# Optimization experiments

Hardware: AMD Instinct MI355X
Metric: run time of the kernel (lower is better)

The kernel has to match this reference:

```python
import jax, jax.numpy as jnp
import numpy as np

B, N, D, E, FF, K = 2, 1024, 768, 8, 4, 2
H = D * FF  # 3072


def _xavier_uniform(key, shape, gain=1.0):
    # shape is (..., out, in) like torch Linear weight; fan_in/out from last two dims
    fan_out, fan_in = shape[-2], shape[-1]
    limit = gain * np.sqrt(6.0 / (fan_in + fan_out))
    return jax.random.uniform(key, shape, jnp.float32, -limit, limit)


def setup_inputs() -> dict:
    key = jax.random.key(0)
    ks = jax.random.split(key, 5)
    tokens = jax.random.normal(ks[0], (B, N, D), jnp.float32)
    # Token-choice top-K routing: softmax over experts, keep top-K weights
    logits = jax.random.normal(ks[1], (B, N, E), jnp.float32)
    probs = jax.nn.softmax(logits, axis=-1)
    topv, topi = jax.lax.top_k(probs, K)              # (B,N,K)
    onehot = jax.nn.one_hot(topi, E, dtype=jnp.float32)  # (B,N,K,E)
    combine_weights = jnp.einsum('bnk,bnke->bne', topv, onehot)  # (B,N,E)
    dispatch_weights = (combine_weights > 0).astype(jnp.float32)
    # Stacked expert weights (torch Linear convention: W is (out, in), y = x @ W.T)
    Wg = _xavier_uniform(ks[2], (E, H, D))
    Wv = _xavier_uniform(ks[3], (E, H, D))
    Wo = _xavier_uniform(ks[4], (E, D, H), gain=0.02)
    scale = jnp.full((E,), 1.0 / E, jnp.float32)  # output_scale init = 1/E
    return dict(tokens=tokens, dispatch_weights=dispatch_weights,
                combine_weights=combine_weights, Wg=Wg, Wv=Wv, Wo=Wo, scale=scale)


def reference(tokens, dispatch_weights, combine_weights, Wg, Wv, Wo, scale):
    Bb, Nn, Dd = tokens.shape
    Ee = Wg.shape[0]
    x = tokens.reshape(Bb * Nn, Dd)                    # (T, D)
    mask = (dispatch_weights.reshape(-1, Ee) > 0).astype(x.dtype)  # (T, E)
    comb = combine_weights.reshape(-1, Ee) * mask      # zero where not dispatched
    # SwiGLU-style expert FFN, all experts in one grouped contraction
    gate = jax.nn.gelu(jnp.einsum('td,ehd->teh', x, Wg), approximate=False)  # (T,E,H)
    value = jnp.einsum('td,ehd->teh', x, Wv)           # (T,E,H)
    expert_out = jnp.einsum('teh,edh->ted', gate * value, Wo) * scale[None, :, None]  # (T,E,D)
    # Weighted combine: sum_e comb[t,e] * expert_out[t,e,:]
    y = jnp.einsum('ted,te->td', expert_out, comb)     # (T, D)
    return y.reshape(Bb, Nn, Dd)
```

## Files before the change

### kernel.cpp

```cpp
#include <hip/hip_runtime.h>
#include <hip/hip_bf16.h>
#include <math.h>

#define T_TOK 2048
#define DIM   768
#define NEXP  8
#define HDIM  3072
#define MAXP  (T_TOK * 2)
#define LDST  40
#define NTILE_MAX 40

typedef __attribute__((ext_vector_type(8))) short bfrag;
typedef __attribute__((ext_vector_type(4))) float f32x4;

__device__ __forceinline__ unsigned short f2bf(float f) {
  union { float f; unsigned int u; } x; x.f = f;
  unsigned int r = x.u + 0x7fffu + ((x.u >> 16) & 1u);
  return (unsigned short)(r >> 16);
}

__global__ void k_route(const float* __restrict__ disp,
                        const float* __restrict__ comb,
                        int* __restrict__ meta,
                        float* __restrict__ row_comb,
                        int* __restrict__ row_token,
                        int* __restrict__ tok2pair) {
  __shared__ int s_cnt[NEXP], s_off[NEXP], s_cur[NEXP];
  __shared__ int s_tn[T_TOK];
  int tid = threadIdx.x;
  if (tid < NEXP) s_cnt[tid] = 0;
  for (int t = tid; t < T_TOK; t += 256) s_tn[t] = 0;
  __syncthreads();
  for (int t = tid; t < T_TOK; t += 256)
    for (int e = 0; e < NEXP; ++e)
      if (disp[t * NEXP + e] > 0.f) atomicAdd(&s_cnt[e], 1);
  __syncthreads();
  if (tid == 0) {
    int acc = 0;
    for (int e = 0; e < NEXP; ++e) { s_off[e] = acc; acc += s_cnt[e]; }
  }
  __syncthreads();
  if (tid < NEXP) {
    s_cur[tid] = s_off[tid];
    meta[tid] = s_cnt[tid];
    meta[NEXP + tid] = s_off[tid];
  }
  __syncthreads();
  for (int t = tid; t < T_TOK; t += 256)
    for (int e = 0; e < NEXP; ++e)
      if (disp[t * NEXP + e] > 0.f) {
        int p = atomicAdd(&s_cur[e], 1);
        row_token[p] = t;
        row_comb[p] = comb[t * NEXP + e];
        int sl = atomicAdd(&s_tn[t], 1);
        tok2pair[t * 2 + sl] = p;
      }
  __syncthreads();
  if (tid == 0) {
    int nt = 0;
    for (int e = 0; e < NEXP; ++e)
      for (int m0 = 0; m0 < s_cnt[e]; m0 += 128)
        meta[17 + nt++] = (e << 16) | (m0 >> 7);
    meta[16] = nt;
  }
}

__global__ void k_xbf(const float* __restrict__ X, unsigned short* __restrict__ Xb) {
  size_t i = ((size_t)blockIdx.x * 256 + threadIdx.x) * 8;
  float4 a = *(const float4*)(X + i);
  float4 b = *(const float4*)(X + i + 4);
  unsigned short r[8];
  r[0]=f2bf(a.x); r[1]=f2bf(a.y); r[2]=f2bf(a.z); r[3]=f2bf(a.w);
  r[4]=f2bf(b.x); r[5]=f2bf(b.y); r[6]=f2bf(b.z); r[7]=f2bf(b.w);
  *(uint4*)(Xb + i) = *(uint4*)r;
}

__global__ __launch_bounds__(256, 2) void k_gemm_gv(
    const unsigned short* __restrict__ Xb,
    const float* __restrict__ Wg,
    const float* __restrict__ Wv,
    const int* __restrict__ meta,
    const int* __restrict__ row_token,
    unsigned short* __restrict__ ubuf)
{
  int blk = blockIdx.x;
  int t = blk % NTILE_MAX;
  int nt = blk / NTILE_MAX;
  if (t >= meta[16]) return;
  int tv = meta[17 + t];
  int e = tv >> 16, m0 = (tv & 0xffff) << 7;
  int cnt = meta[e], off = meta[NEXP + e];
  int n0 = nt * 128;

  __shared__ unsigned short As[128 * LDST];
  __shared__ unsigned short Bgs[128 * LDST];
  __shared__ unsigned short Bvs[128 * LDST];

  int tid = threadIdx.x;
  int wid = tid >> 6, lane = tid & 63;
  int wm = (wid >> 1) * 64, wn = (wid & 1) * 64;
  int lr = lane & 15, quad = lane >> 4;

  int a_tok[2];
#pragma unroll
  for (int r = 0; r < 2; ++r) {
    int row = (tid + 256 * r) >> 2;
    int gr = m0 + row; if (gr >= cnt) gr = cnt - 1;
    a_tok[r] = row_token[off + gr];
  }

  const float* Wgb = Wg + (size_t)e * ((size_t)HDIM * DIM);
  const float* Wvb = Wv + (size_t)e * ((size_t)HDIM * DIM);

  f32x4 zero4 = {0.f, 0.f, 0.f, 0.f};
  f32x4 accg[4][4], accv[4][4];
#pragma unroll
  for (int i = 0; i < 4; ++i)
#pragma unroll
    for (int j = 0; j < 4; ++j) { accg[i][j] = zero4; accv[i][j] = zero4; }

  for (int k0 = 0; k0 < DIM; k0 += 32) {
    __syncthreads();
#pragma unroll
    for (int r = 0; r < 2; ++r) {
      int c = tid + 256 * r;
      int row = c >> 2, sub = c & 3;
      uint4 av = *(const uint4*)(Xb + (size_t)a_tok[r] * DIM + k0 + sub * 8);
      *(uint4*)(&As[row * LDST + sub * 8]) = av;
    }
#pragma unroll
    for (int r = 0; r < 4; ++r) {
      int c = tid + 256 * r;
      int row = c >> 3, c4 = c & 7;
      float4 gv = *(const float4*)(Wgb + (size_t)(n0 + row) * DIM + k0 + c4 * 4);
      ushort4 gp;
      gp.x = f2bf(gv.x); gp.y = f2bf(gv.y); gp.z = f2bf(gv.z); gp.w = f2bf(gv.w);
      *(ushort4*)(&Bgs[row * LDST + c4 * 4]) = gp;
      float4 vv = *(const float4*)(Wvb + (size_t)(n0 + row) * DIM + k0 + c4 * 4);
      ushort4 vp;
      vp.x = f2bf(vv.x); vp.y = f2bf(vv.y); vp.z = f2bf(vv.z); vp.w = f2bf(vv.w);
      *(ushort4*)(&Bvs[row * LDST + c4 * 4]) = vp;
    }
    __syncthreads();
    bfrag a[4], bg[4], bv[4];
#pragma unroll
    for (int i = 0; i < 4; ++i)
      a[i] = *(const bfrag*)(&As[(wm + i * 16 + lr) * LDST + quad * 8]);
#pragma unroll
    for (int j = 0; j < 4; ++j) {
      bg[j] = *(const bfrag*)(&Bgs[(wn + j * 16 + lr) * LDST + quad * 8]);
      bv[j] = *(const bfrag*)(&Bvs[(wn + j * 16 + lr) * LDST + quad * 8]);
    }
#pragma unroll
    for (int i = 0; i < 4; ++i)
#pragma unroll
      for (int j = 0; j < 4; ++j) {
        accg[i][j] = __builtin_amdgcn_mfma_f32_16x16x32_bf16(a[i], bg[j], accg[i][j], 0, 0, 0);
        accv[i][j] = __builtin_amdgcn_mfma_f32_16x16x32_bf16(a[i], bv[j], accv[i][j], 0, 0, 0);
      }
  }

#pragma unroll
  for (int i = 0; i < 4; ++i)
#pragma unroll
    for (int rg = 0; rg < 4; ++rg) {
      int gr = m0 + wm + i * 16 + quad * 4 + rg;
      if (gr < cnt) {
        size_t base = (size_t)(off + gr) * HDIM + n0 + wn;
#pragma unroll
        for (int j = 0; j < 4; ++j) {
          float g = accg[i][j][rg];
          float v = accv[i][j][rg];
          float u = 0.5f * g * (1.0f + erff(g * 0.70710678118654752f)) * v;
          ubuf[base + j * 16 + lr] = f2bf(u);
        }
      }
    }
}

__global__ __launch_bounds__(256, 2) void k_gemm_out(
    const unsigned short* __restrict__ U,
    const float* __restrict__ Wo,
    const float* __restrict__ scale,
    const int* __restrict__ meta,
    const int* __restrict__ row_token,
    const float* __restrict__ row_comb,
    float* __restrict__ partial,
    float* __restrict__ out,
    int mode)
{
  int blk = blockIdx.x;
  int t = blk % NTILE_MAX;
  int rest = blk / NTILE_MAX;
  int nt = rest % 6;
  int ks = rest / 6;
  if (t >= meta[16]) return;
  int tv = meta[17 + t];
  int e = tv >> 16, m0 = (tv & 0xffff) << 7;
  int cnt = meta[e], off = meta[NEXP + e];
  int n0 = nt * 128;
  int kbase = ks * (HDIM / 4);

  __shared__ unsigned short As[128 * LDST];
  __shared__ unsigned short Bs[128 * LDST];

  int tid = threadIdx.x;
  int wid = tid >> 6, lane = tid & 63;
  int wm = (wid >> 1) * 64, wn = (wid & 1) * 64;
  int lr = lane & 15, quad = lane >> 4;

  int a_grow[2];
#pragma unroll
  for (int r = 0; r < 2; ++r) {
    int row = (tid + 256 * r) >> 2;
    int gr = m0 + row; if (gr >= cnt) gr = cnt - 1;
    a_grow[r] = off + gr;
  }

  const float* Wb = Wo + (size_t)e * ((size_t)DIM * HDIM);

  f32x4 zero4 = {0.f, 0.f, 0.f, 0.f};
  f32x4 acc[4][4];
#pragma unroll
  for (int i = 0; i < 4; ++i)
#pragma unroll
    for (int j = 0; j < 4; ++j) acc[i][j] = zero4;

  for (int kk = 0; kk < HDIM / 4; kk += 32) {
    int k0 = kbase + kk;
    __syncthreads();
#pragma unroll
    for (int r = 0; r < 2; ++r) {
      int c = tid + 256 * r;
      int row = c >> 2, sub = c & 3;
      uint4 av = *(const uint4*)(U + (size_t)a_grow[r] * HDIM + k0 + sub * 8);
      *(uint4*)(&As[row * LDST + sub * 8]) = av;
    }
#pragma unroll
    for (int r = 0; r < 4; ++r) {
      int c = tid + 256 * r;
      int row = c >> 3, c4 = c & 7;
      float4 bvv = *(const float4*)(Wb + (size_t)(n0 + row) * HDIM + k0 + c4 * 4);
      ushort4 bp;
      bp.x = f2bf(bvv.x); bp.y = f2bf(bvv.y); bp.z = f2bf(bvv.z); bp.w = f2bf(bvv.w);
      *(ushort4*)(&Bs[row * LDST + c4 * 4]) = bp;
    }
    __syncthreads();
    bfrag a[4], b[4];
#pragma unroll
    for (int i = 0; i < 4; ++i)
      a[i] = *(const bfrag*)(&As[(wm + i * 16 + lr) * LDST + quad * 8]);
#pragma unroll
    for (int j = 0; j < 4; ++j)
      b[j] = *(const bfrag*)(&Bs[(wn + j * 16 + lr) * LDST + quad * 8]);
#pragma unroll
    for (int i = 0; i < 4; ++i)
#pragma unroll
      for (int j = 0; j < 4; ++j)
        acc[i][j] = __builtin_amdgcn_mfma_f32_16x16x32_bf16(a[i], b[j], acc[i][j], 0, 0, 0);
  }

  float sc = scale[e];
#pragma unroll
  for (int i = 0; i < 4; ++i)
#pragma unroll
    for (int rg = 0; rg < 4; ++rg) {
      int gr = m0 + wm + i * 16 + quad * 4 + rg;
      if (gr < cnt) {
        int grow = off + gr;
        float w = row_comb[grow] * sc;
        if (mode == 0) {
          float* pb = partial + ((size_t)ks * MAXP + grow) * DIM + n0 + wn;
#pragma unroll
          for (int j = 0; j < 4; ++j)
            pb[j * 16 + lr] = acc[i][j][rg] * w;
        } else {
          int tok = row_token[grow];
          float* ob = out + (size_t)tok * DIM + n0 + wn;
#pragma unroll
          for (int j = 0; j < 4; ++j)
            atomicAdd(ob + j * 16 + lr, acc[i][j][rg] * w);
        }
      }
    }
}

__global__ void k_combine(const float* __restrict__ partial,
                          const int* __restrict__ tok2pair,
                          float* __restrict__ out) {
  int idx = blockIdx.x * 256 + threadIdx.x;
  int t = idx / 192, d4 = idx % 192;
  int p0 = tok2pair[t * 2], p1 = tok2pair[t * 2 + 1];
  float sx = 0.f, sy = 0.f, sz = 0.f, sw = 0.f;
#pragma unroll
  for (int ks = 0; ks < 4; ++ks) {
    float4 a = *(const float4*)(partial + ((size_t)ks * MAXP + p0) * DIM + d4 * 4);
    float4 b = *(const float4*)(partial + ((size_t)ks * MAXP + p1) * DIM + d4 * 4);
    sx += a.x + b.x; sy += a.y + b.y; sz += a.z + b.z; sw += a.w + b.w;
  }
  float4 r; r.x = sx; r.y = sy; r.z = sz; r.w = sw;
  *(float4*)(out + (size_t)t * DIM + d4 * 4) = r;
}

extern "C" void kernel_launch(void* const* d_in, const int* in_sizes, int n_in,
                              void* d_out, int out_size, void* d_ws, size_t ws_size,
                              hipStream_t stream) {
  const float* tokens = (const float*)d_in[0];
  const float* disp   = (const float*)d_in[1];
  const float* comb   = (const float*)d_in[2];
  const float* Wg     = (const float*)d_in[3];
  const float* Wv     = (const float*)d_in[4];
  const float* Wo     = (const float*)d_in[5];
  const float* scale  = (const float*)d_in[6];
  float* out = (float*)d_out;

  char* ws = (char*)d_ws;
  int*   meta      = (int*)ws;
  int*   row_token = (int*)(ws + 16384);
  float* row_comb  = (float*)(ws + 32768);
  int*   tok2pair  = (int*)(ws + 49152);
  unsigned short* Xb   = (unsigned short*)(ws + (1u << 20));
  unsigned short* ubuf = (unsigned short*)(ws + (5u << 20));
  float* partial = (float*)(ws + (32ull << 20));
  size_t need_partial = (32ull << 20) + (size_t)4 * MAXP * DIM * sizeof(float);
  int mode = (ws_size >= need_partial) ? 0 : 1;

  hipLaunchKernelGGL(k_route, dim3(1), dim3(256), 0, stream,
                     disp, comb, meta, row_comb, row_token, tok2pair);
  hipLaunchKernelGGL(k_xbf, dim3((T_TOK * DIM) / (256 * 8)), dim3(256), 0, stream,
                     tokens, Xb);
  hipLaunchKernelGGL(k_gemm_gv, dim3(NTILE_MAX * 24), dim3(256), 0, stream,
                     Xb, Wg, Wv, meta, row_token, ubuf);
  if (mode == 1)
    hipMemsetAsync(d_out, 0, (size_t)out_size * sizeof(float), stream);
  hipLaunchKernelGGL(k_gemm_out, dim3(NTILE_MAX * 6 * 4), dim3(256), 0, stream,
                     ubuf, Wo, scale, meta, row_token, row_comb, partial, out, mode);
  if (mode == 0)
    hipLaunchKernelGGL(k_combine, dim3((T_TOK * DIM / 4) / 256), dim3(256), 0, stream,
                       partial, tok2pair, out);
}
```

Measured before the change: 422.7 us.

## Pre-convert expert weights to bf16 and stage GEMM tiles with async LDS loads

```diff
diff --git a/kernel.cpp b/kernel.cpp
--- a/kernel.cpp
+++ b/kernel.cpp
@@ -17,6 +17,12 @@
   union { float f; unsigned int u; } x; x.f = f;
   unsigned int r = x.u + 0x7fffu + ((x.u >> 16) & 1u);
   return (unsigned short)(r >> 16);
+}
+
+__device__ __forceinline__ void async16(const void* g, void* l) {
+  __builtin_amdgcn_global_load_lds(
+      (const __attribute__((address_space(1))) void*)g,
+      (__attribute__((address_space(3))) void*)l, 16, 0, 0);
 }
 
 __global__ void k_route(const float* __restrict__ disp,
@@ -65,20 +71,30 @@
   }
 }
 
-__global__ void k_xbf(const float* __restrict__ X, unsigned short* __restrict__ Xb) {
-  size_t i = ((size_t)blockIdx.x * 256 + threadIdx.x) * 8;
-  float4 a = *(const float4*)(X + i);
-  float4 b = *(const float4*)(X + i + 4);
+#define CH_X   196608
+#define CH_W   2359296
+__global__ void k_cvt(const float* __restrict__ X, const float* __restrict__ Wg,
+                      const float* __restrict__ Wv, const float* __restrict__ Wo,
+                      unsigned short* __restrict__ Xb, unsigned short* __restrict__ Wgb,
+                      unsigned short* __restrict__ Wvb, unsigned short* __restrict__ Wob) {
+  int c = blockIdx.x * 256 + threadIdx.x;
+  const float* src; unsigned short* dst; size_t idx;
+  if (c < CH_X)                { src = X;  dst = Xb;  idx = (size_t)c * 8; }
+  else if (c < CH_X + CH_W)    { src = Wg; dst = Wgb; idx = (size_t)(c - CH_X) * 8; }
+  else if (c < CH_X + 2*CH_W)  { src = Wv; dst = Wvb; idx = (size_t)(c - CH_X - CH_W) * 8; }
+  else                         { src = Wo; dst = Wob; idx = (size_t)(c - CH_X - 2*CH_W) * 8; }
+  float4 a = *(const float4*)(src + idx);
+  float4 b = *(const float4*)(src + idx + 4);
   unsigned short r[8];
   r[0]=f2bf(a.x); r[1]=f2bf(a.y); r[2]=f2bf(a.z); r[3]=f2bf(a.w);
   r[4]=f2bf(b.x); r[5]=f2bf(b.y); r[6]=f2bf(b.z); r[7]=f2bf(b.w);
-  *(uint4*)(Xb + i) = *(uint4*)r;
-}
-
-__global__ __launch_bounds__(256, 2) void k_gemm_gv(
+  *(uint4*)(dst + idx) = *(uint4*)r;
+}
+
+__global__ __launch_bounds__(256, 2) void k_gemm_gv_a(
     const unsigned short* __restrict__ Xb,
-    const float* __restrict__ Wg,
-    const float* __restrict__ Wv,
+    const unsigned short* __restrict__ Wgb,
+    const unsigned short* __restrict__ Wvb,
     const int* __restrict__ meta,
     const int* __restrict__ row_token,
     unsigned short* __restrict__ ubuf)
@@ -92,25 +108,26 @@
   int cnt = meta[e], off = meta[NEXP + e];
   int n0 = nt * 128;
 
-  __shared__ unsigned short As[128 * LDST];
-  __shared__ unsigned short Bgs[128 * LDST];
-  __shared__ unsigned short Bvs[128 * LDST];
+  __shared__ unsigned short As[128 * 32];
+  __shared__ unsigned short Bgs[128 * 32];
+  __shared__ unsigned short Bvs[128 * 32];
 
   int tid = threadIdx.x;
   int wid = tid >> 6, lane = tid & 63;
   int wm = (wid >> 1) * 64, wn = (wid & 1) * 64;
   int lr = lane & 15, quad = lane >> 4;
 
-  int a_tok[2];
+  int a_tok[2]; int sub[2]; int brow[2];
 #pragma unroll
   for (int r = 0; r < 2; ++r) {
-    int row = (tid + 256 * r) >> 2;
+    int c = tid + 256 * r;
+    int row = c >> 2; sub[r] = c & 3; brow[r] = row;
     int gr = m0 + row; if (gr >= cnt) gr = cnt - 1;
     a_tok[r] = row_token[off + gr];
   }
 
-  const float* Wgb = Wg + (size_t)e * ((size_t)HDIM * DIM);
-  const float* Wvb = Wv + (size_t)e * ((size_t)HDIM * DIM);
+  const unsigned short* WgB = Wgb + (size_t)e * HDIM * DIM;
+  const unsigned short* WvB = Wvb + (size_t)e * HDIM * DIM;
 
   f32x4 zero4 = {0.f, 0.f, 0.f, 0.f};
   f32x4 accg[4][4], accv[4][4];
@@ -124,32 +141,19 @@
 #pragma unroll
     for (int r = 0; r < 2; ++r) {
       int c = tid + 256 * r;
-      int row = c >> 2, sub = c & 3;
-      uint4 av = *(const uint4*)(Xb + (size_t)a_tok[r] * DIM + k0 + sub * 8);
-      *(uint4*)(&As[row * LDST + sub * 8]) = av;
-    }
-#pragma unroll
-    for (int r = 0; r < 4; ++r) {
-      int c = tid + 256 * r;
-      int row = c >> 3, c4 = c & 7;
-      float4 gv = *(const float4*)(Wgb + (size_t)(n0 + row) * DIM + k0 + c4 * 4);
-      ushort4 gp;
-      gp.x = f2bf(gv.x); gp.y = f2bf(gv.y); gp.z = f2bf(gv.z); gp.w = f2bf(gv.w);
-      *(ushort4*)(&Bgs[row * LDST + c4 * 4]) = gp;
-      float4 vv = *(const float4*)(Wvb + (size_t)(n0 + row) * DIM + k0 + c4 * 4);
-      ushort4 vp;
-      vp.x = f2bf(vv.x); vp.y = f2bf(vv.y); vp.z = f2bf(vv.z); vp.w = f2bf(vv.w);
-      *(ushort4*)(&Bvs[row * LDST + c4 * 4]) = vp;
+      async16(Xb + (size_t)a_tok[r] * DIM + k0 + sub[r] * 8, &As[c * 8]);
+      async16(WgB + (size_t)(n0 + brow[r]) * DIM + k0 + sub[r] * 8, &Bgs[c * 8]);
+      async16(WvB + (size_t)(n0 + brow[r]) * DIM + k0 + sub[r] * 8, &Bvs[c * 8]);
     }
     __syncthreads();
     bfrag a[4], bg[4], bv[4];
 #pragma unroll
     for (int i = 0; i < 4; ++i)
-      a[i] = *(const bfrag*)(&As[(wm + i * 16 + lr) * LDST + quad * 8]);
+      a[i] = *(const bfrag*)(&As[(wm + i * 16 + lr) * 32 + quad * 8]);
 #pragma unroll
     for (int j = 0; j < 4; ++j) {
-      bg[j] = *(const bfrag*)(&Bgs[(wn + j * 16 + lr) * LDST + quad * 8]);
-      bv[j] = *(const bfrag*)(&Bvs[(wn + j * 16 + lr) * LDST + quad * 8]);
+      bg[j] = *(const bfrag*)(&Bgs[(wn + j * 16 + lr) * 32 + quad * 8]);
+      bv[j] = *(const bfrag*)(&Bvs[(wn + j * 16 + lr) * 32 + quad * 8]);
     }
 #pragma unroll
     for (int i = 0; i < 4; ++i)
@@ -178,16 +182,13 @@
     }
 }
 
-__global__ __launch_bounds__(256, 2) void k_gemm_out(
+__global__ __launch_bounds__(256, 2) void k_gemm_out_a(
     const unsigned short* __restrict__ U,
-    const float* __restrict__ Wo,
+    const unsigned short* __restrict__ Wob,
     const float* __restrict__ scale,
     const int* __restrict__ meta,
-    const int* __restrict__ row_token,
     const float* __restrict__ row_comb,
-    float* __restrict__ partial,
-    float* __restrict__ out,
-    int mode)
+    float* __restrict__ partial)
 {
   int blk = blockIdx.x;
   int t = blk % NTILE_MAX;
@@ -201,14 +202,212 @@
   int n0 = nt * 128;
   int kbase = ks * (HDIM / 4);
 
-  __shared__ unsigned short As[128 * LDST];
-  __shared__ unsigned short Bs[128 * LDST];
+  __shared__ unsigned short As[128 * 32];
+  __shared__ unsigned short Bs[128 * 32];
 
   int tid = threadIdx.x;
   int wid = tid >> 6, lane = tid & 63;
   int wm = (wid >> 1) * 64, wn = (wid & 1) * 64;
   int lr = lane & 15, quad = lane >> 4;
 
+  int a_grow[2]; int sub[2]; int brow[2];
+#pragma unroll
+  for (int r = 0; r < 2; ++r) {
+    int c = tid + 256 * r;
+    int row = c >> 2; sub[r] = c & 3; brow[r] = row;
+    int gr = m0 + row; if (gr >= cnt) gr = cnt - 1;
+    a_grow[r] = off + gr;
+  }
+
+  const unsigned short* WoB = Wob + (size_t)e * DIM * HDIM;
+
+  f32x4 zero4 = {0.f, 0.f, 0.f, 0.f};
+  f32x4 acc[4][4];
+#pragma unroll
+  for (int i = 0; i < 4; ++i)
+#pragma unroll
+    for (int j = 0; j < 4; ++j) acc[i][j] = zero4;
+
+  for (int kk = 0; kk < HDIM / 4; kk += 32) {
+    int k0 = kbase + kk;
+    __syncthreads();
+#pragma unroll
+    for (int r = 0; r < 2; ++r) {
+      int c = tid + 256 * r;
+      async16(U + (size_t)a_grow[r] * HDIM + k0 + sub[r] * 8, &As[c * 8]);
+      async16(WoB + (size_t)(n0 + brow[r]) * HDIM + k0 + sub[r] * 8, &Bs[c * 8]);
+    }
+    __syncthreads();
+    bfrag a[4], b[4];
+#pragma unroll
+    for (int i = 0; i < 4; ++i)
+      a[i] = *(const bfrag*)(&As[(wm + i * 16 + lr) * 32 + quad * 8]);
+#pragma unroll
+    for (int j = 0; j < 4; ++j)
+      b[j] = *(const bfrag*)(&Bs[(wn + j * 16 + lr) * 32 + quad * 8]);
+#pragma unroll
+    for (int i = 0; i < 4; ++i)
+#pragma unroll
+      for (int j = 0; j < 4; ++j)
+        acc[i][j] = __builtin_amdgcn_mfma_f32_16x16x32_bf16(a[i], b[j], acc[i][j], 0, 0, 0);
+  }
+
+  float sc = scale[e];
+#pragma unroll
+  for (int i = 0; i < 4; ++i)
+#pragma unroll
+    for (int rg = 0; rg < 4; ++rg) {
+      int gr = m0 + wm + i * 16 + quad * 4 + rg;
+      if (gr < cnt) {
+        int grow = off + gr;
+        float w = row_comb[grow] * sc;
+        float* pb = partial + ((size_t)ks * MAXP + grow) * DIM + n0 + wn;
+#pragma unroll
+        for (int j = 0; j < 4; ++j)
+          pb[j * 16 + lr] = acc[i][j][rg] * w;
+      }
+    }
+}
+
+__global__ void k_combine(const float* __restrict__ partial,
+                          const int* __restrict__ tok2pair,
+                          float* __restrict__ out) {
+  int idx = blockIdx.x * 256 + threadIdx.x;
+  int t = idx / 192, d4 = idx % 192;
+  int p0 = tok2pair[t * 2], p1 = tok2pair[t * 2 + 1];
+  float sx = 0.f, sy = 0.f, sz = 0.f, sw = 0.f;
+#pragma unroll
+  for (int ks = 0; ks < 4; ++ks) {
+    float4 a = *(const float4*)(partial + ((size_t)ks * MAXP + p0) * DIM + d4 * 4);
+    float4 b = *(const float4*)(partial + ((size_t)ks * MAXP + p1) * DIM + d4 * 4);
+    sx += a.x + b.x; sy += a.y + b.y; sz += a.z + b.z; sw += a.w + b.w;
+  }
+  float4 r; r.x = sx; r.y = sy; r.z = sz; r.w = sw;
+  *(float4*)(out + (size_t)t * DIM + d4 * 4) = r;
+}
+
+__global__ void k_xbf(const float* __restrict__ X, unsigned short* __restrict__ Xb) {
+  size_t i = ((size_t)blockIdx.x * 256 + threadIdx.x) * 8;
+  float4 a = *(const float4*)(X + i);
+  float4 b = *(const float4*)(X + i + 4);
+  unsigned short r[8];
+  r[0]=f2bf(a.x); r[1]=f2bf(a.y); r[2]=f2bf(a.z); r[3]=f2bf(a.w);
+  r[4]=f2bf(b.x); r[5]=f2bf(b.y); r[6]=f2bf(b.z); r[7]=f2bf(b.w);
+  *(uint4*)(Xb + i) = *(uint4*)r;
+}
+
+__global__ __launch_bounds__(256, 2) void k_gemm_gv_f(
+    const unsigned short* __restrict__ Xb, const float* __restrict__ Wg,
+    const float* __restrict__ Wv, const int* __restrict__ meta,
+    const int* __restrict__ row_token, unsigned short* __restrict__ ubuf) {
+  int blk = blockIdx.x;
+  int t = blk % NTILE_MAX;
+  int nt = blk / NTILE_MAX;
+  if (t >= meta[16]) return;
+  int tv = meta[17 + t];
+  int e = tv >> 16, m0 = (tv & 0xffff) << 7;
+  int cnt = meta[e], off = meta[NEXP + e];
+  int n0 = nt * 128;
+  __shared__ unsigned short As[128 * LDST];
+  __shared__ unsigned short Bgs[128 * LDST];
+  __shared__ unsigned short Bvs[128 * LDST];
+  int tid = threadIdx.x;
+  int wid = tid >> 6, lane = tid & 63;
+  int wm = (wid >> 1) * 64, wn = (wid & 1) * 64;
+  int lr = lane & 15, quad = lane >> 4;
+  int a_tok[2];
+#pragma unroll
+  for (int r = 0; r < 2; ++r) {
+    int row = (tid + 256 * r) >> 2;
+    int gr = m0 + row; if (gr >= cnt) gr = cnt - 1;
+    a_tok[r] = row_token[off + gr];
+  }
+  const float* Wgb = Wg + (size_t)e * HDIM * DIM;
+  const float* Wvb = Wv + (size_t)e * HDIM * DIM;
+  f32x4 zero4 = {0.f,0.f,0.f,0.f};
+  f32x4 accg[4][4], accv[4][4];
+#pragma unroll
+  for (int i = 0; i < 4; ++i)
+#pragma unroll
+    for (int j = 0; j < 4; ++j) { accg[i][j] = zero4; accv[i][j] = zero4; }
+  for (int k0 = 0; k0 < DIM; k0 += 32) {
+    __syncthreads();
+#pragma unroll
+    for (int r = 0; r < 2; ++r) {
+      int c = tid + 256 * r;
+      int row = c >> 2, s4 = c & 3;
+      uint4 av = *(const uint4*)(Xb + (size_t)a_tok[r] * DIM + k0 + s4 * 8);
+      *(uint4*)(&As[row * LDST + s4 * 8]) = av;
+    }
+#pragma unroll
+    for (int r = 0; r < 4; ++r) {
+      int c = tid + 256 * r;
+      int row = c >> 3, c4 = c & 7;
+      float4 gv = *(const float4*)(Wgb + (size_t)(n0 + row) * DIM + k0 + c4 * 4);
+      ushort4 gp; gp.x=f2bf(gv.x); gp.y=f2bf(gv.y); gp.z=f2bf(gv.z); gp.w=f2bf(gv.w);
+      *(ushort4*)(&Bgs[row * LDST + c4 * 4]) = gp;
+      float4 vv = *(const float4*)(Wvb + (size_t)(n0 + row) * DIM + k0 + c4 * 4);
+      ushort4 vp; vp.x=f2bf(vv.x); vp.y=f2bf(vv.y); vp.z=f2bf(vv.z); vp.w=f2bf(vv.w);
+      *(ushort4*)(&Bvs[row * LDST + c4 * 4]) = vp;
+    }
+    __syncthreads();
+    bfrag a[4], bg[4], bv[4];
+#pragma unroll
+    for (int i = 0; i < 4; ++i)
+      a[i] = *(const bfrag*)(&As[(wm + i * 16 + lr) * LDST + quad * 8]);
+#pragma unroll
+    for (int j = 0; j < 4; ++j) {
+      bg[j] = *(const bfrag*)(&Bgs[(wn + j * 16 + lr) * LDST + quad * 8]);
+      bv[j] = *(const bfrag*)(&Bvs[(wn + j * 16 + lr) * LDST + quad * 8]);
+    }
+#pragma unroll
+    for (int i = 0; i < 4; ++i)
+#pragma unroll
+      for (int j = 0; j < 4; ++j) {
+        accg[i][j] = __builtin_amdgcn_mfma_f32_16x16x32_bf16(a[i], bg[j], accg[i][j], 0, 0, 0);
+        accv[i][j] = __builtin_amdgcn_mfma_f32_16x16x32_bf16(a[i], bv[j], accv[i][j], 0, 0, 0);
+      }
+  }
+#pragma unroll
+  for (int i = 0; i < 4; ++i)
+#pragma unroll
+    for (int rg = 0; rg < 4; ++rg) {
+      int gr = m0 + wm + i * 16 + quad * 4 + rg;
+      if (gr < cnt) {
+        size_t base = (size_t)(off + gr) * HDIM + n0 + wn;
+#pragma unroll
+        for (int j = 0; j < 4; ++j) {
+          float g = accg[i][j][rg];
+          float v = accv[i][j][rg];
+          float u = 0.5f * g * (1.0f + erff(g * 0.70710678118654752f)) * v;
+          ubuf[base + j * 16 + lr] = f2bf(u);
+        }
+      }
+    }
+}
+
+__global__ __launch_bounds__(256, 2) void k_gemm_out_f(
+    const unsigned short* __restrict__ U, const float* __restrict__ Wo,
+    const float* __restrict__ scale, const int* __restrict__ meta,
+    const int* __restrict__ row_token, const float* __restrict__ row_comb,
+    float* __restrict__ partial, float* __restrict__ out, int mode) {
+  int blk = blockIdx.x;
+  int t = blk % NTILE_MAX;
+  int rest = blk / NTILE_MAX;
+  int nt = rest % 6;
+  int ks = rest / 6;
+  if (t >= meta[16]) return;
+  int tv = meta[17 + t];
+  int e = tv >> 16, m0 = (tv & 0xffff) << 7;
+  int cnt = meta[e], off = meta[NEXP + e];
+  int n0 = nt * 128;
+  int kbase = ks * (HDIM / 4);
+  __shared__ unsigned short As[128 * LDST];
+  __shared__ unsigned short Bs[128 * LDST];
+  int tid = threadIdx.x;
+  int wid = tid >> 6, lane = tid & 63;
+  int wm = (wid >> 1) * 64, wn = (wid & 1) * 64;
+  int lr = lane & 15, quad = lane >> 4;
   int a_grow[2];
 #pragma unroll
   for (int r = 0; r < 2; ++r) {
@@ -216,33 +415,29 @@
     int gr = m0 + row; if (gr >= cnt) gr = cnt - 1;
     a_grow[r] = off + gr;
   }
-
-  const float* Wb = Wo + (size_t)e * ((size_t)DIM * HDIM);
-
-  f32x4 zero4 = {0.f, 0.f, 0.f, 0.f};
+  const float* Wb = Wo + (size_t)e * DIM * HDIM;
+  f32x4 zero4 = {0.f,0.f,0.f,0.f};
   f32x4 acc[4][4];
 #pragma unroll
   for (int i = 0; i < 4; ++i)
 #pragma unroll
     for (int j = 0; j < 4; ++j) acc[i][j] = zero4;
-
   for (int kk = 0; kk < HDIM / 4; kk += 32) {
     int k0 = kbase + kk;
     __syncthreads();
 #pragma unroll
     for (int r = 0; r < 2; ++r) {
       int c = tid + 256 * r;
-      int row = c >> 2, sub = c & 3;
-      uint4 av = *(const uint4*)(U + (size_t)a_grow[r] * HDIM + k0 + sub * 8);
-      *(uint4*)(&As[row * LDST + sub * 8]) = av;
+      int row = c >> 2, s4 = c & 3;
+      uint4 av = *(const uint4*)(U + (size_t)a_grow[r] * HDIM + k0 + s4 * 8);
+      *(uint4*)(&As[row * LDST + s4 * 8]) = av;
     }
 #pragma unroll
     for (int r = 0; r < 4; ++r) {
       int c = tid + 256 * r;
       int row = c >> 3, c4 = c & 7;
       float4 bvv = *(const float4*)(Wb + (size_t)(n0 + row) * HDIM + k0 + c4 * 4);
-      ushort4 bp;
-      bp.x = f2bf(bvv.x); bp.y = f2bf(bvv.y); bp.z = f2bf(bvv.z); bp.w = f2bf(bvv.w);
+      ushort4 bp; bp.x=f2bf(bvv.x); bp.y=f2bf(bvv.y); bp.z=f2bf(bvv.z); bp.w=f2bf(bvv.w);
       *(ushort4*)(&Bs[row * LDST + c4 * 4]) = bp;
     }
     __syncthreads();
@@ -259,7 +454,6 @@
       for (int j = 0; j < 4; ++j)
         acc[i][j] = __builtin_amdgcn_mfma_f32_16x16x32_bf16(a[i], b[j], acc[i][j], 0, 0, 0);
   }
-
   float sc = scale[e];
 #pragma unroll
   for (int i = 0; i < 4; ++i)
@@ -272,34 +466,15 @@
         if (mode == 0) {
           float* pb = partial + ((size_t)ks * MAXP + grow) * DIM + n0 + wn;
 #pragma unroll
-          for (int j = 0; j < 4; ++j)
-            pb[j * 16 + lr] = acc[i][j][rg] * w;
+          for (int j = 0; j < 4; ++j) pb[j * 16 + lr] = acc[i][j][rg] * w;
         } else {
           int tok = row_token[grow];
           float* ob = out + (size_t)tok * DIM + n0 + wn;
 #pragma unroll
-          for (int j = 0; j < 4; ++j)
-            atomicAdd(ob + j * 16 + lr, acc[i][j][rg] * w);
+          for (int j = 0; j < 4; ++j) atomicAdd(ob + j * 16 + lr, acc[i][j][rg] * w);
         }
       }
     }
-}
-
-__global__ void k_combine(const float* __restrict__ partial,
-                          const int* __restrict__ tok2pair,
-                          float* __restrict__ out) {
-  int idx = blockIdx.x * 256 + threadIdx.x;
-  int t = idx / 192, d4 = idx % 192;
-  int p0 = tok2pair[t * 2], p1 = tok2pair[t * 2 + 1];
-  float sx = 0.f, sy = 0.f, sz = 0.f, sw = 0.f;
-#pragma unroll
-  for (int ks = 0; ks < 4; ++ks) {
-    float4 a = *(const float4*)(partial + ((size_t)ks * MAXP + p0) * DIM + d4 * 4);
-    float4 b = *(const float4*)(partial + ((size_t)ks * MAXP + p1) * DIM + d4 * 4);
-    sx += a.x + b.x; sy += a.y + b.y; sz += a.z + b.z; sw += a.w + b.w;
-  }
-  float4 r; r.x = sx; r.y = sy; r.z = sz; r.w = sw;
-  *(float4*)(out + (size_t)t * DIM + d4 * 4) = r;
 }
 
 extern "C" void kernel_launch(void* const* d_in, const int* in_sizes, int n_in,
@@ -319,23 +494,42 @@
   int*   row_token = (int*)(ws + 16384);
   float* row_comb  = (float*)(ws + 32768);
   int*   tok2pair  = (int*)(ws + 49152);
-  unsigned short* Xb   = (unsigned short*)(ws + (1u << 20));
-  unsigned short* ubuf = (unsigned short*)(ws + (5u << 20));
-  float* partial = (float*)(ws + (32ull << 20));
-  size_t need_partial = (32ull << 20) + (size_t)4 * MAXP * DIM * sizeof(float);
-  int mode = (ws_size >= need_partial) ? 0 : 1;
+
+  const size_t MB = 1ull << 20;
+  unsigned short* Xb   = (unsigned short*)(ws + 1 * MB);
+  unsigned short* ubuf = (unsigned short*)(ws + 4 * MB);
+  unsigned short* Wgb  = (unsigned short*)(ws + 28 * MB);
+  unsigned short* Wvb  = (unsigned short*)(ws + 64 * MB);
+  unsigned short* Wob  = (unsigned short*)(ws + 100 * MB);
+  float* partial_new   = (float*)(ws + 28 * MB);
 
   hipLaunchKernelGGL(k_route, dim3(1), dim3(256), 0, stream,
                      disp, comb, meta, row_comb, row_token, tok2pair);
-  hipLaunchKernelGGL(k_xbf, dim3((T_TOK * DIM) / (256 * 8)), dim3(256), 0, stream,
-                     tokens, Xb);
-  hipLaunchKernelGGL(k_gemm_gv, dim3(NTILE_MAX * 24), dim3(256), 0, stream,
-                     Xb, Wg, Wv, meta, row_token, ubuf);
-  if (mode == 1)
-    hipMemsetAsync(d_out, 0, (size_t)out_size * sizeof(float), stream);
-  hipLaunchKernelGGL(k_gemm_out, dim3(NTILE_MAX * 6 * 4), dim3(256), 0, stream,
-                     ubuf, Wo, scale, meta, row_token, row_comb, partial, out, mode);
-  if (mode == 0)
+
+  if (ws_size >= 136 * MB) {
+    hipLaunchKernelGGL(k_cvt, dim3((CH_X + 3 * CH_W) / 256), dim3(256), 0, stream,
+                       tokens, Wg, Wv, Wo, Xb, Wgb, Wvb, Wob);
+    hipLaunchKernelGGL(k_gemm_gv_a, dim3(NTILE_MAX * 24), dim3(256), 0, stream,
+                       Xb, Wgb, Wvb, meta, row_token, ubuf);
+    hipLaunchKernelGGL(k_gemm_out_a, dim3(NTILE_MAX * 6 * 4), dim3(256), 0, stream,
+                       ubuf, Wob, scale, meta, row_comb, partial_new);
     hipLaunchKernelGGL(k_combine, dim3((T_TOK * DIM / 4) / 256), dim3(256), 0, stream,
-                       partial, tok2pair, out);
-}
+                       partial_new, tok2pair, out);
+  } else {
+    unsigned short* Xb2   = (unsigned short*)(ws + 1 * MB);
+    unsigned short* ubuf2 = (unsigned short*)(ws + 5 * MB);
+    float* partial_old    = (float*)(ws + 32 * MB);
+    size_t need_partial = 32 * MB + (size_t)4 * MAXP * DIM * sizeof(float);
+    int mode = (ws_size >= need_partial) ? 0 : 1;
+    hipLaunchKernelGGL(k_xbf, dim3((T_TOK * DIM) / (256 * 8)), dim3(256), 0, stream, tokens, Xb2);
+    hipLaunchKernelGGL(k_gemm_gv_f, dim3(NTILE_MAX * 24), dim3(256), 0, stream,
+                       Xb2, Wg, Wv, meta, row_token, ubuf2);
+    if (mode == 1)
+      hipMemsetAsync(d_out, 0, (size_t)out_size * sizeof(float), stream);
+    hipLaunchKernelGGL(k_gemm_out_f, dim3(NTILE_MAX * 6 * 4), dim3(256), 0, stream,
+                       ubuf2, Wo, scale, meta, row_token, row_comb, partial_old, out, mode);
+    if (mode == 0)
+      hipLaunchKernelGGL(k_combine, dim3((T_TOK * DIM / 4) / 256), dim3(256), 0, stream,
+                         partial_old, tok2pair, out);
+  }
+}
```

Measured after the change: 427.6 us. No clear change (+1.2%).

## Keep converted expert weight slices resident in LDS and loop over token tiles

Applied to the files above, without the earlier changes.

```diff
diff --git a/kernel.cpp b/kernel.cpp
--- a/kernel.cpp
+++ b/kernel.cpp
@@ -1,5 +1,4 @@
 #include <hip/hip_runtime.h>
-#include <hip/hip_bf16.h>
 #include <math.h>
 
 #define T_TOK 2048
@@ -7,8 +6,7 @@
 #define NEXP  8
 #define HDIM  3072
 #define MAXP  (T_TOK * 2)
-#define LDST  40
-#define NTILE_MAX 40
+#define BSTR  776
 
 typedef __attribute__((ext_vector_type(8))) short bfrag;
 typedef __attribute__((ext_vector_type(4))) float f32x4;
@@ -17,6 +15,12 @@
   union { float f; unsigned int u; } x; x.f = f;
   unsigned int r = x.u + 0x7fffu + ((x.u >> 16) & 1u);
   return (unsigned short)(r >> 16);
+}
+
+__device__ __forceinline__ void async16(const void* g, void* l) {
+  __builtin_amdgcn_global_load_lds(
+      (const __attribute__((address_space(1))) void*)g,
+      (__attribute__((address_space(3))) void*)l, 16, 0, 0);
 }
 
 __global__ void k_route(const float* __restrict__ disp,
@@ -29,9 +33,9 @@
   __shared__ int s_tn[T_TOK];
   int tid = threadIdx.x;
   if (tid < NEXP) s_cnt[tid] = 0;
-  for (int t = tid; t < T_TOK; t += 256) s_tn[t] = 0;
+  for (int t = tid; t < T_TOK; t += 1024) s_tn[t] = 0;
   __syncthreads();
-  for (int t = tid; t < T_TOK; t += 256)
+  for (int t = tid; t < T_TOK; t += 1024)
     for (int e = 0; e < NEXP; ++e)
       if (disp[t * NEXP + e] > 0.f) atomicAdd(&s_cnt[e], 1);
   __syncthreads();
@@ -46,7 +50,7 @@
     meta[NEXP + tid] = s_off[tid];
   }
   __syncthreads();
-  for (int t = tid; t < T_TOK; t += 256)
+  for (int t = tid; t < T_TOK; t += 1024)
     for (int e = 0; e < NEXP; ++e)
       if (disp[t * NEXP + e] > 0.f) {
         int p = atomicAdd(&s_cur[e], 1);
@@ -55,17 +59,9 @@
         int sl = atomicAdd(&s_tn[t], 1);
         tok2pair[t * 2 + sl] = p;
       }
-  __syncthreads();
-  if (tid == 0) {
-    int nt = 0;
-    for (int e = 0; e < NEXP; ++e)
-      for (int m0 = 0; m0 < s_cnt[e]; m0 += 128)
-        meta[17 + nt++] = (e << 16) | (m0 >> 7);
-    meta[16] = nt;
-  }
-}
-
-__global__ void k_xbf(const float* __restrict__ X, unsigned short* __restrict__ Xb) {
+}
+
+__global__ void k_xcvt(const float* __restrict__ X, unsigned short* __restrict__ Xb) {
   size_t i = ((size_t)blockIdx.x * 256 + threadIdx.x) * 8;
   float4 a = *(const float4*)(X + i);
   float4 b = *(const float4*)(X + i + 4);
@@ -75,7 +71,7 @@
   *(uint4*)(Xb + i) = *(uint4*)r;
 }
 
-__global__ __launch_bounds__(256, 2) void k_gemm_gv(
+__global__ __launch_bounds__(256, 1) void k_gvB(
     const unsigned short* __restrict__ Xb,
     const float* __restrict__ Wg,
     const float* __restrict__ Wv,
@@ -83,206 +79,173 @@
     const int* __restrict__ row_token,
     unsigned short* __restrict__ ubuf)
 {
-  int blk = blockIdx.x;
-  int t = blk % NTILE_MAX;
-  int nt = blk / NTILE_MAX;
-  if (t >= meta[16]) return;
-  int tv = meta[17 + t];
-  int e = tv >> 16, m0 = (tv & 0xffff) << 7;
+  int nt = blockIdx.x;
+  int e  = blockIdx.y;
+  int n0 = nt * 32;
   int cnt = meta[e], off = meta[NEXP + e];
-  int n0 = nt * 128;
-
-  __shared__ unsigned short As[128 * LDST];
-  __shared__ unsigned short Bgs[128 * LDST];
-  __shared__ unsigned short Bvs[128 * LDST];
+  if (cnt <= 0) return;
+
+  __shared__ unsigned short Bg[32 * BSTR];
+  __shared__ unsigned short Bv[32 * BSTR];
+  __shared__ unsigned short As[128 * 128];
 
   int tid = threadIdx.x;
   int wid = tid >> 6, lane = tid & 63;
-  int wm = (wid >> 1) * 64, wn = (wid & 1) * 64;
+  int wm = (wid >> 1) * 64;
+  int wn = (wid & 1) * 16;
   int lr = lane & 15, quad = lane >> 4;
 
-  int a_tok[2];
-#pragma unroll
-  for (int r = 0; r < 2; ++r) {
-    int row = (tid + 256 * r) >> 2;
-    int gr = m0 + row; if (gr >= cnt) gr = cnt - 1;
-    a_tok[r] = row_token[off + gr];
-  }
-
-  const float* Wgb = Wg + (size_t)e * ((size_t)HDIM * DIM);
-  const float* Wvb = Wv + (size_t)e * ((size_t)HDIM * DIM);
-
-  f32x4 zero4 = {0.f, 0.f, 0.f, 0.f};
-  f32x4 accg[4][4], accv[4][4];
-#pragma unroll
-  for (int i = 0; i < 4; ++i)
-#pragma unroll
-    for (int j = 0; j < 4; ++j) { accg[i][j] = zero4; accv[i][j] = zero4; }
-
-  for (int k0 = 0; k0 < DIM; k0 += 32) {
-    __syncthreads();
-#pragma unroll
-    for (int r = 0; r < 2; ++r) {
-      int c = tid + 256 * r;
-      int row = c >> 2, sub = c & 3;
-      uint4 av = *(const uint4*)(Xb + (size_t)a_tok[r] * DIM + k0 + sub * 8);
-      *(uint4*)(&As[row * LDST + sub * 8]) = av;
+  const float* WgB = Wg + ((size_t)e * HDIM + n0) * DIM;
+  const float* WvB = Wv + ((size_t)e * HDIM + n0) * DIM;
+  for (int c = tid; c < 32 * 192; c += 256) {
+    int row = c / 192, k4 = c % 192;
+    float4 g = *(const float4*)(WgB + (size_t)row * DIM + k4 * 4);
+    ushort4 gp; gp.x=f2bf(g.x); gp.y=f2bf(g.y); gp.z=f2bf(g.z); gp.w=f2bf(g.w);
+    *(ushort4*)(&Bg[row * BSTR + k4 * 4]) = gp;
+    float4 v = *(const float4*)(WvB + (size_t)row * DIM + k4 * 4);
+    ushort4 vp; vp.x=f2bf(v.x); vp.y=f2bf(v.y); vp.z=f2bf(v.z); vp.w=f2bf(v.w);
+    *(ushort4*)(&Bv[row * BSTR + k4 * 4]) = vp;
+  }
+
+  int koff = (((tid & 15) ^ (tid >> 4)) * 8);
+  int mt_n = (cnt + 127) >> 7;
+
+  for (int mt = 0; mt < mt_n; ++mt) {
+    int m0 = mt << 7;
+    int tok[8];
+#pragma unroll
+    for (int r = 0; r < 8; ++r) {
+      int row = (tid >> 4) + 16 * r;
+      int gr = m0 + row; if (gr >= cnt) gr = cnt - 1;
+      tok[r] = row_token[off + gr];
     }
-#pragma unroll
-    for (int r = 0; r < 4; ++r) {
-      int c = tid + 256 * r;
-      int row = c >> 3, c4 = c & 7;
-      float4 gv = *(const float4*)(Wgb + (size_t)(n0 + row) * DIM + k0 + c4 * 4);
-      ushort4 gp;
-      gp.x = f2bf(gv.x); gp.y = f2bf(gv.y); gp.z = f2bf(gv.z); gp.w = f2bf(gv.w);
-      *(ushort4*)(&Bgs[row * LDST + c4 * 4]) = gp;
-      float4 vv = *(const float4*)(Wvb + (size_t)(n0 + row) * DIM + k0 + c4 * 4);
-      ushort4 vp;
-      vp.x = f2bf(vv.x); vp.y = f2bf(vv.y); vp.z = f2bf(vv.z); vp.w = f2bf(vv.w);
-      *(ushort4*)(&Bvs[row * LDST + c4 * 4]) = vp;
+    f32x4 zero4 = {0.f, 0.f, 0.f, 0.f};
+    f32x4 accg[4], accv[4];
+#pragma unroll
+    for (int i = 0; i < 4; ++i) { accg[i] = zero4; accv[i] = zero4; }
+
+    for (int k0 = 0; k0 < DIM; k0 += 128) {
+      __syncthreads();
+#pragma unroll
+      for (int r = 0; r < 8; ++r)
+        async16(Xb + (size_t)tok[r] * DIM + k0 + koff, &As[(tid + 256 * r) * 8]);
+      __syncthreads();
+#pragma unroll
+      for (int h = 0; h < 4; ++h) {
+        bfrag bg = *(const bfrag*)(&Bg[(wn + lr) * BSTR + k0 + h * 32 + quad * 8]);
+        bfrag bv = *(const bfrag*)(&Bv[(wn + lr) * BSTR + k0 + h * 32 + quad * 8]);
+        int kc = (h * 4 + quad);
+#pragma unroll
+        for (int i = 0; i < 4; ++i) {
+          int m = wm + i * 16 + lr;
+          bfrag a = *(const bfrag*)(&As[m * 128 + (kc ^ lr) * 8]);
+          accg[i] = __builtin_amdgcn_mfma_f32_16x16x32_bf16(a, bg, accg[i], 0, 0, 0);
+          accv[i] = __builtin_amdgcn_mfma_f32_16x16x32_bf16(a, bv, accv[i], 0, 0, 0);
+        }
+      }
     }
-    __syncthreads();
-    bfrag a[4], bg[4], bv[4];
+
 #pragma unroll
     for (int i = 0; i < 4; ++i)
-      a[i] = *(const bfrag*)(&As[(wm + i * 16 + lr) * LDST + quad * 8]);
-#pragma unroll
-    for (int j = 0; j < 4; ++j) {
-      bg[j] = *(const bfrag*)(&Bgs[(wn + j * 16 + lr) * LDST + quad * 8]);
-      bv[j] = *(const bfrag*)(&Bvs[(wn + j * 16 + lr) * LDST + quad * 8]);
-    }
-#pragma unroll
-    for (int i = 0; i < 4; ++i)
-#pragma unroll
-      for (int j = 0; j < 4; ++j) {
-        accg[i][j] = __builtin_amdgcn_mfma_f32_16x16x32_bf16(a[i], bg[j], accg[i][j], 0, 0, 0);
-        accv[i][j] = __builtin_amdgcn_mfma_f32_16x16x32_bf16(a[i], bv[j], accv[i][j], 0, 0, 0);
-      }
-  }
-
-#pragma unroll
-  for (int i = 0; i < 4; ++i)
-#pragma unroll
-    for (int rg = 0; rg < 4; ++rg) {
-      int gr = m0 + wm + i * 16 + quad * 4 + rg;
-      if (gr < cnt) {
-        size_t base = (size_t)(off + gr) * HDIM + n0 + wn;
-#pragma unroll
-        for (int j = 0; j < 4; ++j) {
-          float g = accg[i][j][rg];
-          float v = accv[i][j][rg];
+#pragma unroll
+      for (int rg = 0; rg < 4; ++rg) {
+        int gr = m0 + wm + i * 16 + quad * 4 + rg;
+        if (gr < cnt) {
+          float g = accg[i][rg];
+          float v = accv[i][rg];
           float u = 0.5f * g * (1.0f + erff(g * 0.70710678118654752f)) * v;
-          ubuf[base + j * 16 + lr] = f2bf(u);
+          ubuf[(size_t)(off + gr) * HDIM + n0 + wn + lr] = f2bf(u);
         }
       }
-    }
-}
-
-__global__ __launch_bounds__(256, 2) void k_gemm_out(
+  }
+}
+
+__global__ __launch_bounds__(256, 1) void k_outB(
     const unsigned short* __restrict__ U,
     const float* __restrict__ Wo,
     const float* __restrict__ scale,
     const int* __restrict__ meta,
-    const int* __restrict__ row_token,
     const float* __restrict__ row_comb,
-    float* __restrict__ partial,
-    float* __restrict__ out,
-    int mode)
+    float* __restrict__ partial)
 {
-  int blk = blockIdx.x;
-  int t = blk % NTILE_MAX;
-  int rest = blk / NTILE_MAX;
-  int nt = rest % 6;
-  int ks = rest / 6;
-  if (t >= meta[16]) return;
-  int tv = meta[17 + t];
-  int e = tv >> 16, m0 = (tv & 0xffff) << 7;
+  int x = blockIdx.x;
+  int nt = x >> 2, ks = x & 3;
+  int e  = blockIdx.y;
+  int n0 = nt * 64;
+  int kb = ks * 768;
   int cnt = meta[e], off = meta[NEXP + e];
-  int n0 = nt * 128;
-  int kbase = ks * (HDIM / 4);
-
-  __shared__ unsigned short As[128 * LDST];
-  __shared__ unsigned short Bs[128 * LDST];
+  if (cnt <= 0) return;
+
+  __shared__ unsigned short Bs[64 * BSTR];
+  __shared__ unsigned short As[128 * 128];
 
   int tid = threadIdx.x;
   int wid = tid >> 6, lane = tid & 63;
-  int wm = (wid >> 1) * 64, wn = (wid & 1) * 64;
+  int wm = (wid >> 1) * 64;
+  int wn = (wid & 1) * 32;
   int lr = lane & 15, quad = lane >> 4;
 
-  int a_grow[2];
-#pragma unroll
-  for (int r = 0; r < 2; ++r) {
-    int row = (tid + 256 * r) >> 2;
-    int gr = m0 + row; if (gr >= cnt) gr = cnt - 1;
-    a_grow[r] = off + gr;
-  }
-
-  const float* Wb = Wo + (size_t)e * ((size_t)DIM * HDIM);
-
-  f32x4 zero4 = {0.f, 0.f, 0.f, 0.f};
-  f32x4 acc[4][4];
-#pragma unroll
-  for (int i = 0; i < 4; ++i)
-#pragma unroll
-    for (int j = 0; j < 4; ++j) acc[i][j] = zero4;
-
-  for (int kk = 0; kk < HDIM / 4; kk += 32) {
-    int k0 = kbase + kk;
-    __syncthreads();
-#pragma unroll
-    for (int r = 0; r < 2; ++r) {
-      int c = tid + 256 * r;
-      int row = c >> 2, sub = c & 3;
-      uint4 av = *(const uint4*)(U + (size_t)a_grow[r] * HDIM + k0 + sub * 8);
-      *(uint4*)(&As[row * LDST + sub * 8]) = av;
+  const float* WoB = Wo + ((size_t)e * DIM + n0) * HDIM + kb;
+  for (int c = tid; c < 64 * 192; c += 256) {
+    int row = c / 192, k4 = c % 192;
+    float4 b = *(const float4*)(WoB + (size_t)row * HDIM + k4 * 4);
+    ushort4 bp; bp.x=f2bf(b.x); bp.y=f2bf(b.y); bp.z=f2bf(b.z); bp.w=f2bf(b.w);
+    *(ushort4*)(&Bs[row * BSTR + k4 * 4]) = bp;
+  }
+
+  int koff = (((tid & 15) ^ (tid >> 4)) * 8);
+  int mt_n = (cnt + 127) >> 7;
+  float sc = scale[e];
+
+  for (int mt = 0; mt < mt_n; ++mt) {
+    int m0 = mt << 7;
+    int arow[8];
+#pragma unroll
+    for (int r = 0; r < 8; ++r) {
+      int row = (tid >> 4) + 16 * r;
+      int gr = m0 + row; if (gr >= cnt) gr = cnt - 1;
+      arow[r] = off + gr;
     }
-#pragma unroll
-    for (int r = 0; r < 4; ++r) {
-      int c = tid + 256 * r;
-      int row = c >> 3, c4 = c & 7;
-      float4 bvv = *(const float4*)(Wb + (size_t)(n0 + row) * HDIM + k0 + c4 * 4);
-      ushort4 bp;
-      bp.x = f2bf(bvv.x); bp.y = f2bf(bvv.y); bp.z = f2bf(bvv.z); bp.w = f2bf(bvv.w);
-      *(ushort4*)(&Bs[row * LDST + c4 * 4]) = bp;
+    f32x4 zero4 = {0.f, 0.f, 0.f, 0.f};
+    f32x4 acc[4][2];
+#pragma unroll
+    for (int i = 0; i < 4; ++i) { acc[i][0] = zero4; acc[i][1] = zero4; }
+
+    for (int k0 = 0; k0 < 768; k0 += 128) {
+      __syncthreads();
+#pragma unroll
+      for (int r = 0; r < 8; ++r)
+        async16(U + (size_t)arow[r] * HDIM + kb + k0 + koff, &As[(tid + 256 * r) * 8]);
+      __syncthreads();
+#pragma unroll
+      for (int h = 0; h < 4; ++h) {
+        bfrag b0 = *(const bfrag*)(&Bs[(wn + lr) * BSTR + k0 + h * 32 + quad * 8]);
+        bfrag b1 = *(const bfrag*)(&Bs[(wn + 16 + lr) * BSTR + k0 + h * 32 + quad * 8]);
+        int kc = (h * 4 + quad);
+#pragma unroll
+        for (int i = 0; i < 4; ++i) {
+          int m = wm + i * 16 + lr;
+          bfrag a = *(const bfrag*)(&As[m * 128 + (kc ^ lr) * 8]);
+          acc[i][0] = __builtin_amdgcn_mfma_f32_16x16x32_bf16(a, b0, acc[i][0], 0, 0, 0);
+          acc[i][1] = __builtin_amdgcn_mfma_f32_16x16x32_bf16(a, b1, acc[i][1], 0, 0, 0);
+        }
+      }
     }
-    __syncthreads();
-    bfrag a[4], b[4];
+
 #pragma unroll
     for (int i = 0; i < 4; ++i)
-      a[i] = *(const bfrag*)(&As[(wm + i * 16 + lr) * LDST + quad * 8]);
-#pragma unroll
-    for (int j = 0; j < 4; ++j)
-      b[j] = *(const bfrag*)(&Bs[(wn + j * 16 + lr) * LDST + quad * 8]);
-#pragma unroll
-    for (int i = 0; i < 4; ++i)
-#pragma unroll
-      for (int j = 0; j < 4; ++j)
-        acc[i][j] = __builtin_amdgcn_mfma_f32_16x16x32_bf16(a[i], b[j], acc[i][j], 0, 0, 0);
-  }
-
-  float sc = scale[e];
-#pragma unroll
-  for (int i = 0; i < 4; ++i)
-#pragma unroll
-    for (int rg = 0; rg < 4; ++rg) {
-      int gr = m0 + wm + i * 16 + quad * 4 + rg;
-      if (gr < cnt) {
-        int grow = off + gr;
-        float w = row_comb[grow] * sc;
-        if (mode == 0) {
-          float* pb = partial + ((size_t)ks * MAXP + grow) * DIM + n0 + wn;
-#pragma unroll
-          for (int j = 0; j < 4; ++j)
-            pb[j * 16 + lr] = acc[i][j][rg] * w;
-        } else {
-          int tok = row_token[grow];
-          float* ob = out + (size_t)tok * DIM + n0 + wn;
-#pragma unroll
-          for (int j = 0; j < 4; ++j)
-            atomicAdd(ob + j * 16 + lr, acc[i][j][rg] * w);
+#pragma unroll
+      for (int rg = 0; rg < 4; ++rg) {
+        int gr = m0 + wm + i * 16 + quad * 4 + rg;
+        if (gr < cnt) {
+          int p = off + gr;
+          float w = row_comb[p] * sc;
+          float* pb = partial + ((size_t)ks * MAXP + p) * DIM + n0;
+          pb[wn + lr]      = acc[i][0][rg] * w;
+          pb[wn + 16 + lr] = acc[i][1][rg] * w;
         }
       }
-    }
+  }
 }
 
 __global__ void k_combine(const float* __restrict__ partial,
@@ -314,28 +277,24 @@
   const float* scale  = (const float*)d_in[6];
   float* out = (float*)d_out;
 
+  const size_t MB = 1ull << 20;
   char* ws = (char*)d_ws;
   int*   meta      = (int*)ws;
   int*   row_token = (int*)(ws + 16384);
   float* row_comb  = (float*)(ws + 32768);
   int*   tok2pair  = (int*)(ws + 49152);
-  unsigned short* Xb   = (unsigned short*)(ws + (1u << 20));
-  unsigned short* ubuf = (unsigned short*)(ws + (5u << 20));
-  float* partial = (float*)(ws + (32ull << 20));
-  size_t need_partial = (32ull << 20) + (size_t)4 * MAXP * DIM * sizeof(float);
-  int mode = (ws_size >= need_partial) ? 0 : 1;
-
-  hipLaunchKernelGGL(k_route, dim3(1), dim3(256), 0, stream,
+  unsigned short* Xb   = (unsigned short*)(ws + 1 * MB);
+  unsigned short* ubuf = (unsigned short*)(ws + 4 * MB);
+  float* partial       = (float*)(ws + 28 * MB);
+
+  hipLaunchKernelGGL(k_route, dim3(1), dim3(1024), 0, stream,
                      disp, comb, meta, row_comb, row_token, tok2pair);
-  hipLaunchKernelGGL(k_xbf, dim3((T_TOK * DIM) / (256 * 8)), dim3(256), 0, stream,
+  hipLaunchKernelGGL(k_xcvt, dim3((T_TOK * DIM) / (256 * 8)), dim3(256), 0, stream,
                      tokens, Xb);
-  hipLaunchKernelGGL(k_gemm_gv, dim3(NTILE_MAX * 24), dim3(256), 0, stream,
+  hipLaunchKernelGGL(k_gvB, dim3(HDIM / 32, NEXP), dim3(256), 0, stream,
                      Xb, Wg, Wv, meta, row_token, ubuf);
-  if (mode == 1)
-    hipMemsetAsync(d_out, 0, (size_t)out_size * sizeof(float), stream);
-  hipLaunchKernelGGL(k_gemm_out, dim3(NTILE_MAX * 6 * 4), dim3(256), 0, stream,
-                     ubuf, Wo, scale, meta, row_token, row_comb, partial, out, mode);
-  if (mode == 0)
-    hipLaunchKernelGGL(k_combine, dim3((T_TOK * DIM / 4) / 256), dim3(256), 0, stream,
-                       partial, tok2pair, out);
-}
+  hipLaunchKernelGGL(k_outB, dim3((DIM / 64) * 4, NEXP), dim3(256), 0, stream,
+                     ubuf, Wo, scale, meta, row_comb, partial);
+  hipLaunchKernelGGL(k_combine, dim3((T_TOK * DIM / 4) / 256), dim3(256), 0, stream,
+                     partial, tok2pair, out);
+}
```

After: 494.7 us. +17.0%, slower.
